# Kernel optimization log

Hardware: AMD Instinct MI355X
Metric: run time of the kernel (lower is better)

Reference implementation:

```python
import jax, jax.numpy as jnp
import numpy as np

N = 50000      # nodes
E = 400000     # edges (before self-loops)
F_IN = 256     # input_dim
HID = 64       # hidden_dim (per-head)
H = 4          # heads
OUT = 16       # output_dim
NEG_SLOPE = 0.2


def _gat_layer(x, W, a_src, a_dst, b, src, dst):
    # x: [N, Fin], W: [Fin, H*HID], a_src/a_dst: [H, HID], b: [H*HID]
    n = x.shape[0]
    h = (x @ W).reshape(n, H, HID)                        # [N,H,D]
    es = jnp.einsum('nhd,hd->nh', h, a_src)               # [N,H]
    ed = jnp.einsum('nhd,hd->nh', h, a_dst)               # [N,H]
    e = jax.nn.leaky_relu(es[src] + ed[dst], NEG_SLOPE)   # [E,H]
    m = jax.ops.segment_max(e, dst, num_segments=n)       # [N,H] segment softmax (stable)
    m = jnp.where(jnp.isfinite(m), m, 0.0)
    p = jnp.exp(e - m[dst])
    s = jax.ops.segment_sum(p, dst, num_segments=n)
    alpha = p / (s[dst] + 1e-16)                          # [E,H]
    out = jax.ops.segment_sum(h[src] * alpha[:, :, None], dst, num_segments=n)  # [N,H,D]
    return out.reshape(n, H * HID) + b


def setup_inputs() -> dict:
    key = jax.random.key(0)
    ks = jax.random.split(key, 24)
    lin = lambda k, i, o: (jax.random.normal(k, (i, o), jnp.float32) / np.sqrt(i)).astype(jnp.float32)
    att = lambda k: (jax.random.normal(k, (H, HID), jnp.float32) * 0.1).astype(jnp.float32)
    FH = H * HID  # 256
    inp = {
        'x': jax.random.normal(ks[0], (N, F_IN), jnp.float32),
        'edge_index': jax.random.randint(ks[1], (2, E), 0, N, dtype=jnp.int64),
        'W1': lin(ks[2], F_IN, FH), 'a1_src': att(ks[3]), 'a1_dst': att(ks[4]), 'b1': jnp.zeros((FH,), jnp.float32),
        'W2': lin(ks[5], FH, FH),   'a2_src': att(ks[6]), 'a2_dst': att(ks[7]), 'b2': jnp.zeros((FH,), jnp.float32),
        'W3': lin(ks[8], FH, FH),   'a3_src': att(ks[9]), 'a3_dst': att(ks[10]), 'b3': jnp.zeros((FH,), jnp.float32),
        'pW1': lin(ks[11], FH, HID), 'pb1': jnp.zeros((HID,), jnp.float32),
        'pW2': lin(ks[12], HID, HID), 'pb2': jnp.zeros((HID,), jnp.float32),
        'cW1': lin(ks[13], FH, HID), 'cb1': jnp.zeros((HID,), jnp.float32),
        'cW2': lin(ks[14], HID, OUT), 'cb2': jnp.zeros((OUT,), jnp.float32),
    }
    return inp


def reference(x, edge_index, W1, a1_src, a1_dst, b1, W2, a2_src, a2_dst, b2,
              W3, a3_src, a3_dst, b3, pW1, pb1, pW2, pb2, cW1, cb1, cW2, cb2):
    n = x.shape[0]
    loop = jnp.arange(n, dtype=edge_index.dtype)          # PyG GATConv adds self-loops
    src = jnp.concatenate([edge_index[0], loop])
    dst = jnp.concatenate([edge_index[1], loop])
    h = jax.nn.elu(_gat_layer(x, W1, a1_src, a1_dst, b1, src, dst))
    h = jax.nn.elu(_gat_layer(h, W2, a2_src, a2_dst, b2, src, dst))
    h = _gat_layer(h, W3, a3_src, a3_dst, b3, src, dst)   # [N, 256]
    logits = jax.nn.relu(h @ cW1 + cb1) @ cW2 + cb2       # classifier (dropout inactive, eval)
    proj = jax.nn.relu(h @ pW1 + pb1) @ pW2 + pb2         # projection head
    return jax.nn.log_softmax(logits, axis=1), proj
```

## Files before the change

### kernel.cpp

```cpp
#include <hip/hip_runtime.h>
#include <hip/hip_bf16.h>

#define NN 50000
#define EE 400000
#define TE (EE + NN)
#define SCAN_B ((NN + 255) / 256)
#define CONV_B (NN * 256 / 4 / 256)
#define PREP_B ((PO_TOTAL + 255) / 256)

typedef float f4 __attribute__((ext_vector_type(4)));
typedef __bf16 b8 __attribute__((ext_vector_type(8)));
typedef unsigned short us8 __attribute__((ext_vector_type(8)));

__device__ __forceinline__ float b2f(unsigned short u) {
    union { unsigned int i; float f; } c; c.i = ((unsigned int)u) << 16; return c.f;
}
__device__ __forceinline__ unsigned short f2b(float x) {
    union { unsigned int i; float f; } c; c.f = x;
    unsigned int i = c.i;
    return (unsigned short)((i + 0x7FFFu + ((i >> 16) & 1u)) >> 16);
}
__device__ __forceinline__ int clampi(int v, int lo, int hi) {
    return v < lo ? lo : (v > hi ? hi : v);
}
__device__ __forceinline__ int uclamp(int v) {
    unsigned u = (unsigned)v;
    return (int)(u < (unsigned)(NN - 1) ? u : (unsigned)(NN - 1));
}

#define PO_WT    0
#define PO_ATT   196608
#define PO_BT    198912
#define PO_BIAS  231680
#define PO_PW2   231808
#define PO_PB2   235904
#define PO_CW2   235968
#define PO_CB2   236992
#define PO_BT2   237008
#define PO_BIAS2 253392
#define PO_TOTAL 253520

__device__ __forceinline__ int detect_xbf(const unsigned int* xw, int tid, int* sm) {
    if (tid < 64) {
        int cnt = 0;
#pragma unroll
        for (int k = 0; k < 4; k++) {
            int i = tid + k * 64;
            unsigned short lo = (unsigned short)(xw[i] & 0xFFFFu);
            int e = (lo >> 7) & 0xFF;
            if (e >= 120 && e <= 132) cnt++;
        }
#pragma unroll
        for (int off = 1; off < 64; off <<= 1) cnt += __shfl_xor(cnt, off, 64);
        if (tid == 0) *sm = (cnt >= 128) ? 1 : 0;
    }
    __syncthreads();
    return *sm;
}
__device__ __forceinline__ int detect_e64(const int* ei, int tid, int* sm) {
    if (tid < 64) {
        int bad = (tid < 16 && ei[2 * tid + 1] != 0) ? 1 : 0;
        unsigned long long anybad = __ballot(bad != 0);
        if (tid == 0) *sm = (anybad == 0ULL) ? 1 : 0;
    }
    __syncthreads();
    return *sm;
}

__device__ __forceinline__ float ldf(const void* p, int i, int bf) {
    return bf ? b2f(((const unsigned short*)p)[i]) : ((const float*)p)[i];
}

__global__ __launch_bounds__(256) void convx_prep_kernel(
    const void* __restrict__ xsrc, unsigned short* __restrict__ dst,
    int* __restrict__ deg, int* __restrict__ cursor,
    const void* W1, const void* W2, const void* W3,
    const void* as1, const void* ad1, const void* b1,
    const void* as2, const void* ad2, const void* b2,
    const void* as3, const void* ad3, const void* b3,
    const void* pW1, const void* pb1, const void* pW2, const void* pb2,
    const void* cW1, const void* cb1, const void* cW2, const void* cb2,
    unsigned short* __restrict__ P) {
    __shared__ int sm;
    int tid = threadIdx.x;
    int bf = detect_xbf((const unsigned int*)xsrc, tid, &sm);
    int b = blockIdx.x;
    if (b < CONV_B) {
        int i = b * 256 + tid;
        if (b < SCAN_B && i < NN) { deg[i] = 0; cursor[i] = 0; }
        if (i >= NN * 256 / 4) return;
        if (bf) {
            ((ushort4*)dst)[i] = ((const ushort4*)xsrc)[i];
        } else {
            float4 v = ((const float4*)xsrc)[i];
            ushort4 o; o.x = f2b(v.x); o.y = f2b(v.y); o.z = f2b(v.z); o.w = f2b(v.w);
            ((ushort4*)dst)[i] = o;
        }
        return;
    }
    int idx = (b - CONV_B) * 256 + tid;
    if (idx >= PO_TOTAL) return;
    float v;
    if (idx < PO_ATT) {
        int l = idx / 65536, r = idx % 65536;
        int n = r >> 8, k = r & 255;
        const void* W = (l == 0) ? W1 : (l == 1) ? W2 : W3;
        v = ldf(W, k * 256 + n, bf);
    } else if (idx < PO_BT) {
        int r = idx - PO_ATT;
        int l = r / 768, w = r % 768, which = w >> 8, j = w & 255;
        const void* s;
        if (which == 0) s = (l == 0) ? as1 : (l == 1) ? as2 : as3;
        else if (which == 1) s = (l == 0) ? ad1 : (l == 1) ? ad2 : ad3;
        else s = (l == 0) ? b1 : (l == 1) ? b2 : b3;
        v = ldf(s, j, bf);
    } else if (idx < PO_BIAS) {
        int r3 = idx - PO_BT;
        int r = r3 >> 8, k = r3 & 255;
        v = (r < 64) ? ldf(cW1, k * 64 + r, bf) : ldf(pW1, k * 64 + (r - 64), bf);
    } else if (idx < PO_PW2) {
        int r = idx - PO_BIAS;
        v = (r < 64) ? ldf(cb1, r, bf) : ldf(pb1, r - 64, bf);
    } else if (idx < PO_PB2) {
        v = ldf(pW2, idx - PO_PW2, bf);
    } else if (idx < PO_CW2) {
        v = ldf(pb2, idx - PO_PB2, bf);
    } else if (idx < PO_CB2) {
        v = ldf(cW2, idx - PO_CW2, bf);
    } else if (idx < PO_BT2) {
        v = ldf(cb2, idx - PO_CB2, bf);
    } else if (idx < PO_BIAS2) {
        int r2 = idx - PO_BT2;
        int r = r2 >> 7, k = r2 & 127;
        if (r < 16) v = (k < 64) ? ldf(cW2, k * 16 + r, bf) : 0.f;
        else if (r < 80) v = (k >= 64) ? ldf(pW2, (k - 64) * 64 + (r - 16), bf) : 0.f;
        else v = 0.f;
    } else {
        int r = idx - PO_BIAS2;
        v = (r < 16) ? ldf(cb2, r, bf) : (r < 80 ? ldf(pb2, r - 16, bf) : 0.f);
    }
    P[idx] = f2b(v);
}

__device__ __forceinline__ void edge_decode(const int* __restrict__ ei, int mode64, int e,
                                            int& src, int& dst) {
    if (e < EE) {
        if (mode64) { src = ei[2 * e]; dst = ei[2 * EE + 2 * e]; }
        else        { src = ei[e];     dst = ei[EE + e]; }
        src = clampi(src, 0, NN - 1);
        dst = clampi(dst, 0, NN - 1);
    } else {
        src = dst = e - EE;
    }
}

__global__ __launch_bounds__(256) void deg_kernel(const int* __restrict__ ei,
                                                  int* __restrict__ deg) {
    __shared__ int sm;
    int tid = threadIdx.x;
    int mode64 = detect_e64(ei, tid, &sm);
    int e = blockIdx.x * 256 + tid;
    if (e >= TE) return;
    int src, dst;
    edge_decode(ei, mode64, e, src, dst);
    atomicAdd(&deg[dst], 1);
}

__global__ __launch_bounds__(256) void scanA_kernel(const int* __restrict__ deg,
                                                    int* __restrict__ offs, int* __restrict__ bsum) {
    __shared__ int s[256];
    int t = threadIdx.x, i = blockIdx.x * 256 + t;
    int v = (i < NN) ? deg[i] : 0;
    s[t] = v;
    __syncthreads();
    for (int off = 1; off < 256; off <<= 1) {
        int x = (t >= off) ? s[t - off] : 0;
        __syncthreads();
        s[t] += x;
        __syncthreads();
    }
    if (i < NN) offs[i] = s[t] - v;
    if (t == 255) bsum[blockIdx.x] = s[255];
}
__global__ __launch_bounds__(256) void scanBC_kernel(int* __restrict__ offs,
                                                     const int* __restrict__ bsum) {
    __shared__ int s[256];
    int t = threadIdx.x;
    int v = (t < SCAN_B) ? bsum[t] : 0;
    s[t] = v;
    __syncthreads();
    for (int off = 1; off < 256; off <<= 1) {
        int x = (t >= off) ? s[t - off] : 0;
        __syncthreads();
        s[t] += x;
        __syncthreads();
    }
    int add = (blockIdx.x > 0) ? s[blockIdx.x - 1] : 0;
    int i = blockIdx.x * 256 + t;
    if (i < NN) offs[i] += add;
    if (i == 0) offs[NN] = TE;
}

__global__ __launch_bounds__(256) void scatter_kernel(const int* __restrict__ ei,
                                                      const int* __restrict__ offs,
                                                      int* __restrict__ cursor,
                                                      int* __restrict__ srcs) {
    __shared__ int sm;
    int tid = threadIdx.x;
    int mode64 = detect_e64(ei, tid, &sm);
    int e = blockIdx.x * 256 + tid;
    if (e >= TE) return;
    int src, dst;
    edge_decode(ei, mode64, e, src, dst);
    int pos = atomicAdd(&cursor[dst], 1);
    int slot = offs[dst] + pos;
    if (slot >= 0 && slot < TE) srcs[slot] = src;
}

__device__ __forceinline__ void async_ld16(const unsigned short* g, unsigned short* l) {
    __builtin_amdgcn_global_load_lds(
        (const __attribute__((address_space(1))) unsigned int*)g,
        (__attribute__((address_space(3))) unsigned int*)l, 16, 0, 0);
}

__global__ __launch_bounds__(256) void gemm_bt_kernel(
    const unsigned short* __restrict__ A, const unsigned short* __restrict__ Bt,
    unsigned short* __restrict__ C, int M,
    const unsigned short* __restrict__ asrc, const unsigned short* __restrict__ adst,
    float* __restrict__ es, float* __restrict__ ed) {
    const int K = 256, Nc = 256;
    __shared__ unsigned short As[2][128 * 32];
    __shared__ unsigned short Bs[2][128 * 32];
    int tid = threadIdx.x;
    int lane = tid & 63;
    int wave = tid >> 6;
    int wr = wave >> 1, wc = wave & 1;
    int m0 = blockIdx.x * 128;
    int n0 = blockIdx.y * 128;
    f4 acc[4][4];
#pragma unroll
    for (int i = 0; i < 4; i++)
#pragma unroll
        for (int j = 0; j < 4; j++) acc[i][j] = (f4){0.f, 0.f, 0.f, 0.f};

    int rin = lane >> 2;
    int qsl = lane & 3;
    int qg  = qsl ^ ((rin >> 1) & 3);
    int rsel = lane & 15;
    int q16 = lane >> 4;
    int slotq = q16 ^ ((rsel >> 1) & 3);

    auto stage = [&](int b, int kt) {
#pragma unroll
        for (int t = 0; t < 4; t++) {
            int seg = wave * 4 + t;
            if (seg < 8) {
                int r = seg * 16 + rin;
                int gm = m0 + r;
                if (gm < M)
                    async_ld16(A + (size_t)gm * K + kt + qg * 8, &As[b][seg * 512]);
            } else {
                int r = (seg - 8) * 16 + rin;
                int gn = n0 + r;
                async_ld16(Bt + (size_t)gn * K + kt + qg * 8, &Bs[b][(seg - 8) * 512]);
            }
        }
    };

    const int nk = K >> 5;
    stage(0, 0);
    __syncthreads();
    for (int s = 0; s < nk; s++) {
        int cur = s & 1;
        if (s + 1 < nk) stage(cur ^ 1, (s + 1) << 5);
        b8 af[4], bfv[4];
#pragma unroll
        for (int i = 0; i < 4; i++) {
            af[i]  = *(const b8*)(&As[cur][(wr * 64 + i * 16 + rsel) * 32 + slotq * 8]);
            bfv[i] = *(const b8*)(&Bs[cur][(wc * 64 + i * 16 + rsel) * 32 + slotq * 8]);
        }
#pragma unroll
        for (int i = 0; i < 4; i++)
#pragma unroll
            for (int j = 0; j < 4; j++)
                acc[i][j] = __builtin_amdgcn_mfma_f32_16x16x32_bf16(af[i], bfv[j], acc[i][j], 0, 0, 0);
        __syncthreads();
    }
    int cl = lane & 15, rq = lane >> 4;
    {
        int head = blockIdx.y * 2 + wc;
        float asv[4], adv[4];
#pragma unroll
        for (int j = 0; j < 4; j++) {
            asv[j] = b2f(asrc[head * 64 + j * 16 + cl]);
            adv[j] = b2f(adst[head * 64 + j * 16 + cl]);
        }
#pragma unroll
        for (int i = 0; i < 4; i++) {
            float pes[4], ped[4];
#pragma unroll
            for (int r = 0; r < 4; r++) {
                float se = 0.f, de = 0.f;
#pragma unroll
                for (int j = 0; j < 4; j++) {
                    se += acc[i][j][r] * asv[j];
                    de += acc[i][j][r] * adv[j];
                }
                pes[r] = se; ped[r] = de;
            }
#pragma unroll
            for (int off = 1; off < 16; off <<= 1) {
#pragma unroll
                for (int r = 0; r < 4; r++) {
                    pes[r] += __shfl_xor(pes[r], off, 64);
                    ped[r] += __shfl_xor(ped[r], off, 64);
                }
            }
            if (cl == 0) {
#pragma unroll
                for (int r = 0; r < 4; r++) {
                    int row = m0 + wr * 64 + i * 16 + rq * 4 + r;
                    if (row < M) {
                        es[(size_t)row * 4 + head] = pes[r];
                        ed[(size_t)row * 4 + head] = ped[r];
                    }
                }
            }
        }
    }
#pragma unroll
    for (int j = 0; j < 4; j++) {
        int col = n0 + wc * 64 + j * 16 + cl;
#pragma unroll
        for (int i = 0; i < 4; i++) {
#pragma unroll
            for (int r = 0; r < 4; r++) {
                int row = m0 + wr * 64 + i * 16 + rq * 4 + r;
                if (row < M) C[(size_t)row * Nc + col] = f2b(acc[i][j][r]);
            }
        }
    }
}

__global__ __launch_bounds__(256) void gemm_final_kernel(
    const unsigned short* __restrict__ A, const unsigned short* __restrict__ Bt1,
    const unsigned short* __restrict__ bias1, const unsigned short* __restrict__ B2g,
    const unsigned short* __restrict__ bias2,
    float* __restrict__ flog, float* __restrict__ fproj, int M) {
    const int K = 256;
    __shared__ unsigned short smem[32768];
    unsigned short* As0 = smem;
    unsigned short* Bs0 = smem + 8192;
    unsigned short* T   = smem;
    unsigned short* B2s = smem + 16384;
    int tid = threadIdx.x;
    int lane = tid & 63;
    int wave = tid >> 6;
    int wr = wave >> 1, wc = wave & 1;
    int m0 = blockIdx.x * 128;
    f4 acc[4][4];
#pragma unroll
    for (int i = 0; i < 4; i++)
#pragma unroll
        for (int j = 0; j < 4; j++) acc[i][j] = (f4){0.f, 0.f, 0.f, 0.f};

    int rin = lane >> 2;
    int qsl = lane & 3;
    int qg  = qsl ^ ((rin >> 1) & 3);
    int rsel = lane & 15;
    int q16 = lane >> 4;
    int slotq = q16 ^ ((rsel >> 1) & 3);

#pragma unroll
    for (int t = 0; t < 8; t++) {
        int row = t * 16 + wave * 4 + (lane >> 4);
        int chunk = lane & 15;
        async_ld16(B2g + row * 128 + ((chunk ^ (row & 15)) << 3),
                   B2s + (t * 16 + wave * 4) * 128);
    }

    auto stage = [&](int b, int kt) {
#pragma unroll
        for (int t = 0; t < 4; t++) {
            int seg = wave * 4 + t;
            if (seg < 8) {
                int r = seg * 16 + rin;
                int gm = m0 + r;
                if (gm < M)
                    async_ld16(A + (size_t)gm * K + kt + qg * 8, &As0[b * 4096 + seg * 512]);
            } else {
                int r = (seg - 8) * 16 + rin;
                async_ld16(Bt1 + (size_t)r * K + kt + qg * 8, &Bs0[b * 4096 + (seg - 8) * 512]);
            }
        }
    };

    stage(0, 0);
    __syncthreads();
    for (int s = 0; s < 8; s++) {
        int cur = s & 1;
        if (s + 1 < 8) stage(cur ^ 1, (s + 1) << 5);
        b8 af[4], bfv[4];
#pragma unroll
        for (int i = 0; i < 4; i++) {
            af[i]  = *(const b8*)(&As0[cur * 4096 + (wr * 64 + i * 16 + rsel) * 32 + slotq * 8]);
            bfv[i] = *(const b8*)(&Bs0[cur * 4096 + (wc * 64 + i * 16 + rsel) * 32 + slotq * 8]);
        }
#pragma unroll
        for (int i = 0; i < 4; i++)
#pragma unroll
            for (int j = 0; j < 4; j++)
                acc[i][j] = __builtin_amdgcn_mfma_f32_16x16x32_bf16(af[i], bfv[j], acc[i][j], 0, 0, 0);
        __syncthreads();
    }

    int cl = lane & 15, rq = lane >> 4;
#pragma unroll
    for (int j = 0; j < 4; j++) {
        int col = wc * 64 + j * 16 + cl;
        float bv = b2f(bias1[col]);
        int chunk = col >> 3, cr = col & 7;
#pragma unroll
        for (int i = 0; i < 4; i++) {
#pragma unroll
            for (int r = 0; r < 4; r++) {
                int row = wr * 64 + i * 16 + rq * 4 + r;
                float v = fmaxf(acc[i][j][r] + bv, 0.0f);
                T[row * 128 + ((chunk ^ (row & 15)) << 3) + cr] = f2b(v);
            }
        }
    }
    __syncthreads();

    f4 acc2[4][4];
#pragma unroll
    for (int i = 0; i < 4; i++)
#pragma unroll
        for (int j = 0; j < 4; j++) acc2[i][j] = (f4){0.f, 0.f, 0.f, 0.f};
#pragma unroll
    for (int s2 = 0; s2 < 4; s2++) {
        int kc = s2 * 4 + q16;
        b8 af2[4], bf2[4];
#pragma unroll
        for (int i = 0; i < 4; i++) {
            int row = wr * 64 + i * 16 + rsel;
            af2[i] = *(const b8*)(&T[row * 128 + ((kc ^ (row & 15)) << 3)]);
        }
#pragma unroll
        for (int j = 0; j < 4; j++) {
            int col = wc * 64 + j * 16 + rsel;
            bf2[j] = *(const b8*)(&B2s[col * 128 + ((kc ^ (col & 15)) << 3)]);
        }
#pragma unroll
        for (int i = 0; i < 4; i++)
#pragma unroll
            for (int j = 0; j < 4; j++)
                acc2[i][j] = __builtin_amdgcn_mfma_f32_16x16x32_bf16(af2[i], bf2[j], acc2[i][j], 0, 0, 0);
    }

#pragma unroll
    for (int i = 0; i < 4; i++) {
#pragma unroll
        for (int r = 0; r < 4; r++) {
            int row = m0 + wr * 64 + i * 16 + rq * 4 + r;
            if (row >= M) continue;
            if (wc == 0) {
                float lv = acc2[i][0][r] + b2f(bias2[cl]);
                float mx = lv;
#pragma unroll
                for (int off = 1; off < 16; off <<= 1) mx = fmaxf(mx, __shfl_xor(mx, off, 64));
                float se = __expf(lv - mx);
#pragma unroll
                for (int off = 1; off < 16; off <<= 1) se += __shfl_xor(se, off, 64);
                flog[(size_t)row * 16 + cl] = lv - mx - __logf(se);
#pragma unroll
                for (int j = 1; j < 4; j++) {
                    float pv = acc2[i][j][r] + b2f(bias2[j * 16 + cl]);
                    fproj[(size_t)row * 64 + j * 16 + cl - 16] = pv;
                }
            } else {
                float pv = acc2[i][0][r] + b2f(bias2[64 + cl]);
                fproj[(size_t)row * 64 + 48 + cl] = pv;
            }
        }
    }
}

__global__ __launch_bounds__(256) void aggr_kernel(
    const unsigned short* __restrict__ H, const float* __restrict__ es,
    const float* __restrict__ ed,
    const int* __restrict__ offs, const int* __restrict__ srcs,
    const unsigned short* __restrict__ bias, unsigned short* __restrict__ out, int N, int elu) {
    int gw = (blockIdx.x * 256 + threadIdx.x) >> 6;
    int lane = threadIdx.x & 63;
    if (gw >= N) return;
    int half = lane >> 5;
    int lh = lane & 31;
    int ch = lh << 3;
    int head = lh >> 3;
    int j0 = clampi(offs[gw], 0, TE);
    int j1 = clampi(offs[gw + 1], j0, TE);
    int d = j1 - j0;
    float edh = ed[gw * 4 + head];
    float a0 = 0.f, a1 = 0.f, a2 = 0.f, a3 = 0.f;
    float a4 = 0.f, a5 = 0.f, a6 = 0.f, a7 = 0.f;
    float sw = 0.f;
    int nfull8 = d & ~7;
    for (int t = 0; t < nfull8; t += 8) {
        int base = j0 + t + half * 4;
        int s0 = uclamp(srcs[base]), s1 = uclamp(srcs[base + 1]);
        int s2 = uclamp(srcs[base + 2]), s3 = uclamp(srcs[base + 3]);
        float e0 = es[s0 * 4 + head], e1 = es[s1 * 4 + head];
        float e2 = es[s2 * 4 + head], e3 = es[s3 * 4 + head];
        us8 h0 = *(const us8*)(H + (size_t)s0 * 256 + ch);
        us8 h1 = *(const us8*)(H + (size_t)s1 * 256 + ch);
        us8 h2 = *(const us8*)(H + (size_t)s2 * 256 + ch);
        us8 h3 = *(const us8*)(H + (size_t)s3 * 256 + ch);
        float v0 = e0 + edh; v0 = v0 > 0.f ? v0 : 0.2f * v0;
        float v1 = e1 + edh; v1 = v1 > 0.f ? v1 : 0.2f * v1;
        float v2 = e2 + edh; v2 = v2 > 0.f ? v2 : 0.2f * v2;
        float v3 = e3 + edh; v3 = v3 > 0.f ? v3 : 0.2f * v3;
        float w0 = __expf(v0), w1 = __expf(v1), w2 = __expf(v2), w3 = __expf(v3);
        sw += (w0 + w1) + (w2 + w3);
        a0 += w0 * b2f(h0[0]) + w1 * b2f(h1[0]) + w2 * b2f(h2[0]) + w3 * b2f(h3[0]);
        a1 += w0 * b2f(h0[1]) + w1 * b2f(h1[1]) + w2 * b2f(h2[1]) + w3 * b2f(h3[1]);
        a2 += w0 * b2f(h0[2]) + w1 * b2f(h1[2]) + w2 * b2f(h2[2]) + w3 * b2f(h3[2]);
        a3 += w0 * b2f(h0[3]) + w1 * b2f(h1[3]) + w2 * b2f(h2[3]) + w3 * b2f(h3[3]);
        a4 += w0 * b2f(h0[4]) + w1 * b2f(h1[4]) + w2 * b2f(h2[4]) + w3 * b2f(h3[4]);
        a5 += w0 * b2f(h0[5]) + w1 * b2f(h1[5]) + w2 * b2f(h2[5]) + w3 * b2f(h3[5]);
        a6 += w0 * b2f(h0[6]) + w1 * b2f(h1[6]) + w2 * b2f(h2[6]) + w3 * b2f(h3[6]);
        a7 += w0 * b2f(h0[7]) + w1 * b2f(h1[7]) + w2 * b2f(h2[7]) + w3 * b2f(h3[7]);
    }
    int jt = j0 + nfull8;
    if (j1 - jt >= 4) {
        int base = jt + half * 2;
        int s0 = uclamp(srcs[base]), s1 = uclamp(srcs[base + 1]);
        float e0 = es[s0 * 4 + head], e1 = es[s1 * 4 + head];
        us8 h0 = *(const us8*)(H + (size_t)s0 * 256 + ch);
        us8 h1 = *(const us8*)(H + (size_t)s1 * 256 + ch);
        float v0 = e0 + edh; v0 = v0 > 0.f ? v0 : 0.2f * v0;
        float v1 = e1 + edh; v1 = v1 > 0.f ? v1 : 0.2f * v1;
        float w0 = __expf(v0), w1 = __expf(v1);
        sw += w0 + w1;
        a0 += w0 * b2f(h0[0]) + w1 * b2f(h1[0]);
        a1 += w0 * b2f(h0[1]) + w1 * b2f(h1[1]);
        a2 += w0 * b2f(h0[2]) + w1 * b2f(h1[2]);
        a3 += w0 * b2f(h0[3]) + w1 * b2f(h1[3]);
        a4 += w0 * b2f(h0[4]) + w1 * b2f(h1[4]);
        a5 += w0 * b2f(h0[5]) + w1 * b2f(h1[5]);
        a6 += w0 * b2f(h0[6]) + w1 * b2f(h1[6]);
        a7 += w0 * b2f(h0[7]) + w1 * b2f(h1[7]);
        jt += 4;
    }
    for (int j = jt + half; j < j1; j += 2) {
        int sA = uclamp(srcs[j]);
        float eA = es[sA * 4 + head];
        us8 hA = *(const us8*)(H + (size_t)sA * 256 + ch);
        float vA = eA + edh; vA = vA > 0.f ? vA : 0.2f * vA;
        float wA = __expf(vA);
        sw += wA;
        a0 += wA * b2f(hA[0]); a1 += wA * b2f(hA[1]);
        a2 += wA * b2f(hA[2]); a3 += wA * b2f(hA[3]);
        a4 += wA * b2f(hA[4]); a5 += wA * b2f(hA[5]);
        a6 += wA * b2f(hA[6]); a7 += wA * b2f(hA[7]);
    }
    sw += __shfl_xor(sw, 32, 64);
    a0 += __shfl_xor(a0, 32, 64); a1 += __shfl_xor(a1, 32, 64);
    a2 += __shfl_xor(a2, 32, 64); a3 += __shfl_xor(a3, 32, 64);
    a4 += __shfl_xor(a4, 32, 64); a5 += __shfl_xor(a5, 32, 64);
    a6 += __shfl_xor(a6, 32, 64); a7 += __shfl_xor(a7, 32, 64);
    if (half == 0) {
        float rs = 1.f / (sw + 1e-16f);
        us8 bv = *(const us8*)(bias + ch);
        float r0 = a0 * rs + b2f(bv[0]), r1 = a1 * rs + b2f(bv[1]);
        float r2 = a2 * rs + b2f(bv[2]), r3 = a3 * rs + b2f(bv[3]);
        float r4 = a4 * rs + b2f(bv[4]), r5 = a5 * rs + b2f(bv[5]);
        float r6 = a6 * rs + b2f(bv[6]), r7 = a7 * rs + b2f(bv[7]);
        if (elu) {
            r0 = r0 > 0.f ? r0 : __expf(r0) - 1.f;
            r1 = r1 > 0.f ? r1 : __expf(r1) - 1.f;
            r2 = r2 > 0.f ? r2 : __expf(r2) - 1.f;
            r3 = r3 > 0.f ? r3 : __expf(r3) - 1.f;
            r4 = r4 > 0.f ? r4 : __expf(r4) - 1.f;
            r5 = r5 > 0.f ? r5 : __expf(r5) - 1.f;
            r6 = r6 > 0.f ? r6 : __expf(r6) - 1.f;
            r7 = r7 > 0.f ? r7 : __expf(r7) - 1.f;
        }
        us8 o;
        o[0] = f2b(r0); o[1] = f2b(r1); o[2] = f2b(r2); o[3] = f2b(r3);
        o[4] = f2b(r4); o[5] = f2b(r5); o[6] = f2b(r6); o[7] = f2b(r7);
        *(us8*)(out + (size_t)gw * 256 + ch) = o;
    }
}

extern "C" void kernel_launch(void* const* d_in, const int* in_sizes, int n_in,
                              void* d_out, int out_size, void* d_ws, size_t ws_size,
                              hipStream_t stream) {
    (void)in_sizes; (void)n_in; (void)out_size; (void)ws_size;
    const int* ei = (const int*)d_in[1];

    char* p = (char*)d_ws;
    auto take = [&](size_t bytes) -> void* {
        void* r = (void*)p;
        p += (bytes + 255) & ~(size_t)255;
        return r;
    };
    int* deg    = (int*)take((size_t)NN * 4);
    int* cursor = (int*)take((size_t)NN * 4);
    int* offs   = (int*)take((size_t)(NN + 1) * 4);
    int* bsum   = (int*)take(256 * 4);
    int* srcs   = (int*)take((size_t)TE * 4);
    float* es   = (float*)take((size_t)NN * 16);
    float* ed   = (float*)take((size_t)NN * 16);
    unsigned short* bufH = (unsigned short*)take((size_t)NN * 256 * 2);
    unsigned short* buf1 = (unsigned short*)take((size_t)NN * 256 * 2);
    unsigned short* buf2 = (unsigned short*)take((size_t)NN * 256 * 2);
    unsigned short* P    = (unsigned short*)take((size_t)PO_TOTAL * 2);
    unsigned short* xb = buf2;

    convx_prep_kernel<<<CONV_B + PREP_B, 256, 0, stream>>>(
        d_in[0], xb, deg, cursor,
        d_in[2], d_in[6], d_in[10],
        d_in[3], d_in[4], d_in[5],
        d_in[7], d_in[8], d_in[9],
        d_in[11], d_in[12], d_in[13],
        d_in[14], d_in[15], d_in[16], d_in[17],
        d_in[18], d_in[19], d_in[20], d_in[21],
        P);

    deg_kernel<<<(TE + 255) / 256, 256, 0, stream>>>(ei, deg);
    scanA_kernel<<<SCAN_B, 256, 0, stream>>>(deg, offs, bsum);
    scanBC_kernel<<<SCAN_B, 256, 0, stream>>>(offs, bsum);
    scatter_kernel<<<(TE + 255) / 256, 256, 0, stream>>>(ei, offs, cursor, srcs);

    const unsigned short* X = xb;
    unsigned short* outbuf[3] = {buf1, buf2, buf1};
    for (int l = 0; l < 3; l++) {
        const unsigned short* Wt  = P + PO_WT + l * 65536;
        const unsigned short* asr = P + PO_ATT + l * 768;
        const unsigned short* adr = P + PO_ATT + l * 768 + 256;
        const unsigned short* bcb = P + PO_ATT + l * 768 + 512;
        gemm_bt_kernel<<<dim3((NN + 127) / 128, 2), 256, 0, stream>>>(
            X, Wt, bufH, NN, asr, adr, es, ed);
        aggr_kernel<<<12500, 256, 0, stream>>>(bufH, es, ed, offs, srcs, bcb, outbuf[l], NN, (l < 2) ? 1 : 0);
        X = outbuf[l];
    }
    float* out0 = (float*)d_out;
    float* out1 = out0 + (size_t)NN * 16;
    gemm_final_kernel<<<(NN + 127) / 128, 256, 0, stream>>>(
        X, P + PO_BT, P + PO_BIAS, P + PO_BT2, P + PO_BIAS2, out0, out1, NN);
}
```

Measured before the change: 405.8 us.

## Fuse graph build and all GAT layers into one cooperative persistent kernel

Replaces the chain of separate launches (degree count, scan, scatter, three GEMM+aggregation pairs, final head) with one cooperative persistent kernel. Grid-wide barriers separate the phases, and blocks loop over virtual tiles. The CSR scatter is overlapped with the first layer's GEMM in the same phase. This removes per-launch overhead and tail gaps, but every phase now waits on grid syncs and occupancy is fixed by launch bounds. The old multi-kernel path stays as a fallback if the cooperative launch fails.

```diff
diff --git a/kernel.cpp b/kernel.cpp
--- a/kernel.cpp
+++ b/kernel.cpp
@@ -1,5 +1,8 @@
 #include <hip/hip_runtime.h>
 #include <hip/hip_bf16.h>
+#include <hip/hip_cooperative_groups.h>
+
+namespace cg = cooperative_groups;
 
 #define NN 50000
 #define EE 400000
@@ -7,6 +10,10 @@
 #define SCAN_B ((NN + 255) / 256)
 #define CONV_B (NN * 256 / 4 / 256)
 #define PREP_B ((PO_TOTAL + 255) / 256)
+#define DEG_B ((TE + 255) / 256)
+#define GEMM_T 782
+#define FIN_T 391
+#define AGGR_B 12500
 
 typedef float f4 __attribute__((ext_vector_type(4)));
 typedef __bf16 b8 __attribute__((ext_vector_type(8)));
@@ -69,6 +76,24 @@
 
 __device__ __forceinline__ float ldf(const void* p, int i, int bf) {
     return bf ? b2f(((const unsigned short*)p)[i]) : ((const float*)p)[i];
+}
+
+__device__ __forceinline__ void async_ld16(const unsigned short* g, unsigned short* l) {
+    __builtin_amdgcn_global_load_lds(
+        (const __attribute__((address_space(1))) unsigned int*)g,
+        (__attribute__((address_space(3))) unsigned int*)l, 16, 0, 0);
+}
+
+__device__ __forceinline__ void edge_decode(const int* __restrict__ ei, int mode64, int e,
+                                            int& src, int& dst) {
+    if (e < EE) {
+        if (mode64) { src = ei[2 * e]; dst = ei[2 * EE + 2 * e]; }
+        else        { src = ei[e];     dst = ei[EE + e]; }
+        src = clampi(src, 0, NN - 1);
+        dst = clampi(dst, 0, NN - 1);
+    } else {
+        src = dst = e - EE;
+    }
 }
 
 __global__ __launch_bounds__(256) void convx_prep_kernel(
@@ -83,8 +108,8 @@
     unsigned short* __restrict__ P) {
     __shared__ int sm;
     int tid = threadIdx.x;
+    int b = blockIdx.x;
     int bf = detect_xbf((const unsigned int*)xsrc, tid, &sm);
-    int b = blockIdx.x;
     if (b < CONV_B) {
         int i = b * 256 + tid;
         if (b < SCAN_B && i < NN) { deg[i] = 0; cursor[i] = 0; }
@@ -142,18 +167,6 @@
     P[idx] = f2b(v);
 }
 
-__device__ __forceinline__ void edge_decode(const int* __restrict__ ei, int mode64, int e,
-                                            int& src, int& dst) {
-    if (e < EE) {
-        if (mode64) { src = ei[2 * e]; dst = ei[2 * EE + 2 * e]; }
-        else        { src = ei[e];     dst = ei[EE + e]; }
-        src = clampi(src, 0, NN - 1);
-        dst = clampi(dst, 0, NN - 1);
-    } else {
-        src = dst = e - EE;
-    }
-}
-
 __global__ __launch_bounds__(256) void deg_kernel(const int* __restrict__ ei,
                                                   int* __restrict__ deg) {
     __shared__ int sm;
@@ -215,12 +228,6 @@
     int pos = atomicAdd(&cursor[dst], 1);
     int slot = offs[dst] + pos;
     if (slot >= 0 && slot < TE) srcs[slot] = src;
-}
-
-__device__ __forceinline__ void async_ld16(const unsigned short* g, unsigned short* l) {
-    __builtin_amdgcn_global_load_lds(
-        (const __attribute__((address_space(1))) unsigned int*)g,
-        (__attribute__((address_space(3))) unsigned int*)l, 16, 0, 0);
 }
 
 __global__ __launch_bounds__(256) void gemm_bt_kernel(
@@ -242,31 +249,24 @@
     for (int i = 0; i < 4; i++)
 #pragma unroll
         for (int j = 0; j < 4; j++) acc[i][j] = (f4){0.f, 0.f, 0.f, 0.f};
-
-    int rin = lane >> 2;
-    int qsl = lane & 3;
+    int rin = lane >> 2, qsl = lane & 3;
     int qg  = qsl ^ ((rin >> 1) & 3);
-    int rsel = lane & 15;
-    int q16 = lane >> 4;
+    int rsel = lane & 15, q16 = lane >> 4;
     int slotq = q16 ^ ((rsel >> 1) & 3);
-
     auto stage = [&](int b, int kt) {
 #pragma unroll
         for (int t = 0; t < 4; t++) {
             int seg = wave * 4 + t;
             if (seg < 8) {
-                int r = seg * 16 + rin;
-                int gm = m0 + r;
+                int gm = m0 + seg * 16 + rin;
                 if (gm < M)
                     async_ld16(A + (size_t)gm * K + kt + qg * 8, &As[b][seg * 512]);
             } else {
-                int r = (seg - 8) * 16 + rin;
-                int gn = n0 + r;
+                int gn = n0 + (seg - 8) * 16 + rin;
                 async_ld16(Bt + (size_t)gn * K + kt + qg * 8, &Bs[b][(seg - 8) * 512]);
             }
         }
     };
-
     const int nk = K >> 5;
     stage(0, 0);
     __syncthreads();
@@ -363,14 +363,10 @@
     for (int i = 0; i < 4; i++)
 #pragma unroll
         for (int j = 0; j < 4; j++) acc[i][j] = (f4){0.f, 0.f, 0.f, 0.f};
-
-    int rin = lane >> 2;
-    int qsl = lane & 3;
+    int rin = lane >> 2, qsl = lane & 3;
     int qg  = qsl ^ ((rin >> 1) & 3);
-    int rsel = lane & 15;
-    int q16 = lane >> 4;
+    int rsel = lane & 15, q16 = lane >> 4;
     int slotq = q16 ^ ((rsel >> 1) & 3);
-
 #pragma unroll
     for (int t = 0; t < 8; t++) {
         int row = t * 16 + wave * 4 + (lane >> 4);
@@ -378,14 +374,12 @@
         async_ld16(B2g + row * 128 + ((chunk ^ (row & 15)) << 3),
                    B2s + (t * 16 + wave * 4) * 128);
     }
-
     auto stage = [&](int b, int kt) {
 #pragma unroll
         for (int t = 0; t < 4; t++) {
             int seg = wave * 4 + t;
             if (seg < 8) {
-                int r = seg * 16 + rin;
-                int gm = m0 + r;
+                int gm = m0 + seg * 16 + rin;
                 if (gm < M)
                     async_ld16(A + (size_t)gm * K + kt + qg * 8, &As0[b * 4096 + seg * 512]);
             } else {
@@ -394,7 +388,6 @@
             }
         }
     };
-
     stage(0, 0);
     __syncthreads();
     for (int s = 0; s < 8; s++) {
@@ -413,7 +406,6 @@
                 acc[i][j] = __builtin_amdgcn_mfma_f32_16x16x32_bf16(af[i], bfv[j], acc[i][j], 0, 0, 0);
         __syncthreads();
     }
-
     int cl = lane & 15, rq = lane >> 4;
 #pragma unroll
     for (int j = 0; j < 4; j++) {
@@ -431,7 +423,6 @@
         }
     }
     __syncthreads();
-
     f4 acc2[4][4];
 #pragma unroll
     for (int i = 0; i < 4; i++)
@@ -457,7 +448,6 @@
             for (int j = 0; j < 4; j++)
                 acc2[i][j] = __builtin_amdgcn_mfma_f32_16x16x32_bf16(af2[i], bf2[j], acc2[i][j], 0, 0, 0);
     }
-
 #pragma unroll
     for (int i = 0; i < 4; i++) {
 #pragma unroll
@@ -593,6 +583,423 @@
     }
 }
 
+__global__ __launch_bounds__(256, 4) void mega_kernel(
+    const int* __restrict__ ei,
+    int* __restrict__ deg, int* __restrict__ cursor,
+    int* __restrict__ offs, int* __restrict__ bsum, int* __restrict__ srcs,
+    float* __restrict__ es, float* __restrict__ ed,
+    unsigned short* __restrict__ bufH, unsigned short* __restrict__ buf1,
+    unsigned short* __restrict__ buf2, const unsigned short* __restrict__ P,
+    float* __restrict__ out_logits, float* __restrict__ out_proj) {
+    __shared__ unsigned short smem[16384];
+    __shared__ int sm0;
+    cg::grid_group grid = cg::this_grid();
+    int tid = threadIdx.x;
+    int m64 = detect_e64(ei, tid, &sm0);
+    const int NB = gridDim.x;
+    int lane = tid & 63, wave = tid >> 6;
+    int wr = wave >> 1, wc = wave & 1;
+    int rin = lane >> 2, qsl = lane & 3;
+    int qg = qsl ^ ((rin >> 1) & 3);
+    int rsel = lane & 15, q16 = lane >> 4;
+    int slotq = q16 ^ ((rsel >> 1) & 3);
+    int cl = lane & 15, rq = lane >> 4;
+
+    auto gemm_tile = [&](int m0, int n0, const unsigned short* A,
+                         const unsigned short* Wt,
+                         const unsigned short* asrc, const unsigned short* adst) {
+        unsigned short* As0 = smem;
+        unsigned short* Bs0 = smem + 8192;
+        const int K = 256;
+        f4 acc[4][4];
+#pragma unroll
+        for (int i = 0; i < 4; i++)
+#pragma unroll
+            for (int j = 0; j < 4; j++) acc[i][j] = (f4){0.f, 0.f, 0.f, 0.f};
+        auto stage = [&](int b, int kt) {
+#pragma unroll
+            for (int t = 0; t < 4; t++) {
+                int seg = wave * 4 + t;
+                if (seg < 8) {
+                    int gm = m0 + seg * 16 + rin;
+                    if (gm < NN)
+                        async_ld16(A + (size_t)gm * K + kt + qg * 8, &As0[b * 4096 + seg * 512]);
+                } else {
+                    int gn = n0 + (seg - 8) * 16 + rin;
+                    async_ld16(Wt + (size_t)gn * K + kt + qg * 8, &Bs0[b * 4096 + (seg - 8) * 512]);
+                }
+            }
+        };
+        stage(0, 0);
+        __syncthreads();
+        for (int s = 0; s < 8; s++) {
+            int cur = s & 1;
+            if (s + 1 < 8) stage(cur ^ 1, (s + 1) << 5);
+            b8 af[4], bfv[4];
+#pragma unroll
+            for (int i = 0; i < 4; i++) {
+                af[i]  = *(const b8*)(&As0[cur * 4096 + (wr * 64 + i * 16 + rsel) * 32 + slotq * 8]);
+                bfv[i] = *(const b8*)(&Bs0[cur * 4096 + (wc * 64 + i * 16 + rsel) * 32 + slotq * 8]);
+            }
+#pragma unroll
+            for (int i = 0; i < 4; i++)
+#pragma unroll
+                for (int j = 0; j < 4; j++)
+                    acc[i][j] = __builtin_amdgcn_mfma_f32_16x16x32_bf16(af[i], bfv[j], acc[i][j], 0, 0, 0);
+            __syncthreads();
+        }
+        int head = (n0 >> 6) + wc;
+        float asv[4], adv[4];
+#pragma unroll
+        for (int j = 0; j < 4; j++) {
+            asv[j] = b2f(asrc[head * 64 + j * 16 + cl]);
+            adv[j] = b2f(adst[head * 64 + j * 16 + cl]);
+        }
+#pragma unroll
+        for (int i = 0; i < 4; i++) {
+            float pes[4], ped[4];
+#pragma unroll
+            for (int r = 0; r < 4; r++) {
+                float se = 0.f, de = 0.f;
+#pragma unroll
+                for (int j = 0; j < 4; j++) {
+                    se += acc[i][j][r] * asv[j];
+                    de += acc[i][j][r] * adv[j];
+                }
+                pes[r] = se; ped[r] = de;
+            }
+#pragma unroll
+            for (int off = 1; off < 16; off <<= 1) {
+#pragma unroll
+                for (int r = 0; r < 4; r++) {
+                    pes[r] += __shfl_xor(pes[r], off, 64);
+                    ped[r] += __shfl_xor(ped[r], off, 64);
+                }
+            }
+            if (cl == 0) {
+#pragma unroll
+                for (int r = 0; r < 4; r++) {
+                    int row = m0 + wr * 64 + i * 16 + rq * 4 + r;
+                    if (row < NN) {
+                        es[(size_t)row * 4 + head] = pes[r];
+                        ed[(size_t)row * 4 + head] = ped[r];
+                    }
+                }
+            }
+        }
+#pragma unroll
+        for (int j = 0; j < 4; j++) {
+            int col = n0 + wc * 64 + j * 16 + cl;
+#pragma unroll
+            for (int i = 0; i < 4; i++) {
+#pragma unroll
+                for (int r = 0; r < 4; r++) {
+                    int row = m0 + wr * 64 + i * 16 + rq * 4 + r;
+                    if (row < NN) bufH[(size_t)row * 256 + col] = f2b(acc[i][j][r]);
+                }
+            }
+        }
+    };
+
+    auto aggr_node = [&](int gw, const unsigned short* bias, unsigned short* out, int elu) {
+        if (gw >= NN) return;
+        int half = lane >> 5;
+        int lh = lane & 31;
+        int ch = lh << 3;
+        int head = lh >> 3;
+        int j0 = clampi(offs[gw], 0, TE);
+        int j1 = clampi(offs[gw + 1], j0, TE);
+        int d = j1 - j0;
+        float edh = ed[gw * 4 + head];
+        float a0 = 0.f, a1 = 0.f, a2 = 0.f, a3 = 0.f;
+        float a4 = 0.f, a5 = 0.f, a6 = 0.f, a7 = 0.f;
+        float sw = 0.f;
+        int nfull8 = d & ~7;
+        for (int t = 0; t < nfull8; t += 8) {
+            int base = j0 + t + half * 4;
+            int s0 = uclamp(srcs[base]), s1 = uclamp(srcs[base + 1]);
+            int s2 = uclamp(srcs[base + 2]), s3 = uclamp(srcs[base + 3]);
+            float e0 = es[s0 * 4 + head], e1 = es[s1 * 4 + head];
+            float e2 = es[s2 * 4 + head], e3 = es[s3 * 4 + head];
+            us8 h0 = *(const us8*)(bufH + (size_t)s0 * 256 + ch);
+            us8 h1 = *(const us8*)(bufH + (size_t)s1 * 256 + ch);
+            us8 h2 = *(const us8*)(bufH + (size_t)s2 * 256 + ch);
+            us8 h3 = *(const us8*)(bufH + (size_t)s3 * 256 + ch);
+            float v0 = e0 + edh; v0 = v0 > 0.f ? v0 : 0.2f * v0;
+            float v1 = e1 + edh; v1 = v1 > 0.f ? v1 : 0.2f * v1;
+            float v2 = e2 + edh; v2 = v2 > 0.f ? v2 : 0.2f * v2;
+            float v3 = e3 + edh; v3 = v3 > 0.f ? v3 : 0.2f * v3;
+            float w0 = __expf(v0), w1 = __expf(v1), w2 = __expf(v2), w3 = __expf(v3);
+            sw += (w0 + w1) + (w2 + w3);
+            a0 += w0 * b2f(h0[0]) + w1 * b2f(h1[0]) + w2 * b2f(h2[0]) + w3 * b2f(h3[0]);
+            a1 += w0 * b2f(h0[1]) + w1 * b2f(h1[1]) + w2 * b2f(h2[1]) + w3 * b2f(h3[1]);
+            a2 += w0 * b2f(h0[2]) + w1 * b2f(h1[2]) + w2 * b2f(h2[2]) + w3 * b2f(h3[2]);
+            a3 += w0 * b2f(h0[3]) + w1 * b2f(h1[3]) + w2 * b2f(h2[3]) + w3 * b2f(h3[3]);
+            a4 += w0 * b2f(h0[4]) + w1 * b2f(h1[4]) + w2 * b2f(h2[4]) + w3 * b2f(h3[4]);
+            a5 += w0 * b2f(h0[5]) + w1 * b2f(h1[5]) + w2 * b2f(h2[5]) + w3 * b2f(h3[5]);
+            a6 += w0 * b2f(h0[6]) + w1 * b2f(h1[6]) + w2 * b2f(h2[6]) + w3 * b2f(h3[6]);
+            a7 += w0 * b2f(h0[7]) + w1 * b2f(h1[7]) + w2 * b2f(h2[7]) + w3 * b2f(h3[7]);
+        }
+        int jt = j0 + nfull8;
+        if (j1 - jt >= 4) {
+            int base = jt + half * 2;
+            int s0 = uclamp(srcs[base]), s1 = uclamp(srcs[base + 1]);
+            float e0 = es[s0 * 4 + head], e1 = es[s1 * 4 + head];
+            us8 h0 = *(const us8*)(bufH + (size_t)s0 * 256 + ch);
+            us8 h1 = *(const us8*)(bufH + (size_t)s1 * 256 + ch);
+            float v0 = e0 + edh; v0 = v0 > 0.f ? v0 : 0.2f * v0;
+            float v1 = e1 + edh; v1 = v1 > 0.f ? v1 : 0.2f * v1;
+            float w0 = __expf(v0), w1 = __expf(v1);
+            sw += w0 + w1;
+            a0 += w0 * b2f(h0[0]) + w1 * b2f(h1[0]);
+            a1 += w0 * b2f(h0[1]) + w1 * b2f(h1[1]);
+            a2 += w0 * b2f(h0[2]) + w1 * b2f(h1[2]);
+            a3 += w0 * b2f(h0[3]) + w1 * b2f(h1[3]);
+            a4 += w0 * b2f(h0[4]) + w1 * b2f(h1[4]);
+            a5 += w0 * b2f(h0[5]) + w1 * b2f(h1[5]);
+            a6 += w0 * b2f(h0[6]) + w1 * b2f(h1[6]);
+            a7 += w0 * b2f(h0[7]) + w1 * b2f(h1[7]);
+            jt += 4;
+        }
+        for (int j = jt + half; j < j1; j += 2) {
+            int sA = uclamp(srcs[j]);
+            float eA = es[sA * 4 + head];
+            us8 hA = *(const us8*)(bufH + (size_t)sA * 256 + ch);
+            float vA = eA + edh; vA = vA > 0.f ? vA : 0.2f * vA;
+            float wA = __expf(vA);
+            sw += wA;
+            a0 += wA * b2f(hA[0]); a1 += wA * b2f(hA[1]);
+            a2 += wA * b2f(hA[2]); a3 += wA * b2f(hA[3]);
+            a4 += wA * b2f(hA[4]); a5 += wA * b2f(hA[5]);
+            a6 += wA * b2f(hA[6]); a7 += wA * b2f(hA[7]);
+        }
+        sw += __shfl_xor(sw, 32, 64);
+        a0 += __shfl_xor(a0, 32, 64); a1 += __shfl_xor(a1, 32, 64);
+        a2 += __shfl_xor(a2, 32, 64); a3 += __shfl_xor(a3, 32, 64);
+        a4 += __shfl_xor(a4, 32, 64); a5 += __shfl_xor(a5, 32, 64);
+        a6 += __shfl_xor(a6, 32, 64); a7 += __shfl_xor(a7, 32, 64);
+        if (half == 0) {
+            float rs = 1.f / (sw + 1e-16f);
+            us8 bv = *(const us8*)(bias + ch);
+            float r0 = a0 * rs + b2f(bv[0]), r1 = a1 * rs + b2f(bv[1]);
+            float r2 = a2 * rs + b2f(bv[2]), r3 = a3 * rs + b2f(bv[3]);
+            float r4 = a4 * rs + b2f(bv[4]), r5 = a5 * rs + b2f(bv[5]);
+            float r6 = a6 * rs + b2f(bv[6]), r7 = a7 * rs + b2f(bv[7]);
+            if (elu) {
+                r0 = r0 > 0.f ? r0 : __expf(r0) - 1.f;
+                r1 = r1 > 0.f ? r1 : __expf(r1) - 1.f;
+                r2 = r2 > 0.f ? r2 : __expf(r2) - 1.f;
+                r3 = r3 > 0.f ? r3 : __expf(r3) - 1.f;
+                r4 = r4 > 0.f ? r4 : __expf(r4) - 1.f;
+                r5 = r5 > 0.f ? r5 : __expf(r5) - 1.f;
+                r6 = r6 > 0.f ? r6 : __expf(r6) - 1.f;
+                r7 = r7 > 0.f ? r7 : __expf(r7) - 1.f;
+            }
+            us8 o;
+            o[0] = f2b(r0); o[1] = f2b(r1); o[2] = f2b(r2); o[3] = f2b(r3);
+            o[4] = f2b(r4); o[5] = f2b(r5); o[6] = f2b(r6); o[7] = f2b(r7);
+            *(us8*)(out + (size_t)gw * 256 + ch) = o;
+        }
+    };
+
+    auto final_tile = [&](int m0) {
+        const unsigned short* A = buf1;
+        const unsigned short* Bt1 = P + PO_BT;
+        const unsigned short* bias1 = P + PO_BIAS;
+        const unsigned short* B2g = P + PO_BT2;
+        const unsigned short* bias2 = P + PO_BIAS2;
+        unsigned short* As0 = smem;
+        unsigned short* Bs0 = smem + 8192;
+        const int K = 256;
+        f4 acc[4][4];
+#pragma unroll
+        for (int i = 0; i < 4; i++)
+#pragma unroll
+            for (int j = 0; j < 4; j++) acc[i][j] = (f4){0.f, 0.f, 0.f, 0.f};
+        auto stage = [&](int b, int kt) {
+#pragma unroll
+            for (int t = 0; t < 4; t++) {
+                int seg = wave * 4 + t;
+                if (seg < 8) {
+                    int gm = m0 + seg * 16 + rin;
+                    if (gm < NN)
+                        async_ld16(A + (size_t)gm * K + kt + qg * 8, &As0[b * 4096 + seg * 512]);
+                } else {
+                    int r = (seg - 8) * 16 + rin;
+                    async_ld16(Bt1 + (size_t)r * K + kt + qg * 8, &Bs0[b * 4096 + (seg - 8) * 512]);
+                }
+            }
+        };
+        stage(0, 0);
+        __syncthreads();
+        for (int s = 0; s < 8; s++) {
+            int cur = s & 1;
+            if (s + 1 < 8) stage(cur ^ 1, (s + 1) << 5);
+            b8 af[4], bfv[4];
+#pragma unroll
+            for (int i = 0; i < 4; i++) {
+                af[i]  = *(const b8*)(&As0[cur * 4096 + (wr * 64 + i * 16 + rsel) * 32 + slotq * 8]);
+                bfv[i] = *(const b8*)(&Bs0[cur * 4096 + (wc * 64 + i * 16 + rsel) * 32 + slotq * 8]);
+            }
+#pragma unroll
+            for (int i = 0; i < 4; i++)
+#pragma unroll
+                for (int j = 0; j < 4; j++)
+                    acc[i][j] = __builtin_amdgcn_mfma_f32_16x16x32_bf16(af[i], bfv[j], acc[i][j], 0, 0, 0);
+            __syncthreads();
+        }
+        unsigned short* T = smem;
+#pragma unroll
+        for (int j = 0; j < 4; j++) {
+            int col = wc * 64 + j * 16 + cl;
+            float bv = b2f(bias1[col]);
+            int chunk = col >> 3, cr = col & 7;
+#pragma unroll
+            for (int i = 0; i < 4; i++) {
+#pragma unroll
+                for (int r = 0; r < 4; r++) {
+                    int row = wr * 64 + i * 16 + rq * 4 + r;
+                    float v = fmaxf(acc[i][j][r] + bv, 0.0f);
+                    T[row * 128 + ((chunk ^ (row & 15)) << 3) + cr] = f2b(v);
+                }
+            }
+        }
+        __syncthreads();
+        f4 acc2[4][4];
+#pragma unroll
+        for (int i = 0; i < 4; i++)
+#pragma unroll
+            for (int j = 0; j < 4; j++) acc2[i][j] = (f4){0.f, 0.f, 0.f, 0.f};
+#pragma unroll
+        for (int s2 = 0; s2 < 4; s2++) {
+            int kc = s2 * 4 + q16;
+            b8 af2[4], bf2[4];
+#pragma unroll
+            for (int i = 0; i < 4; i++) {
+                int row = wr * 64 + i * 16 + rsel;
+                af2[i] = *(const b8*)(&T[row * 128 + ((kc ^ (row & 15)) << 3)]);
+            }
+#pragma unroll
+            for (int j = 0; j < 4; j++) {
+                int col = wc * 64 + j * 16 + rsel;
+                bf2[j] = *(const b8*)(B2g + (size_t)col * 128 + kc * 8);
+            }
+#pragma unroll
+            for (int i = 0; i < 4; i++)
+#pragma unroll
+                for (int j = 0; j < 4; j++)
+                    acc2[i][j] = __builtin_amdgcn_mfma_f32_16x16x32_bf16(af2[i], bf2[j], acc2[i][j], 0, 0, 0);
+        }
+#pragma unroll
+        for (int i = 0; i < 4; i++) {
+#pragma unroll
+            for (int r = 0; r < 4; r++) {
+                int row = m0 + wr * 64 + i * 16 + rq * 4 + r;
+                if (row >= NN) continue;
+                if (wc == 0) {
+                    float lv = acc2[i][0][r] + b2f(bias2[cl]);
+                    float mx = lv;
+#pragma unroll
+                    for (int off = 1; off < 16; off <<= 1) mx = fmaxf(mx, __shfl_xor(mx, off, 64));
+                    float se = __expf(lv - mx);
+#pragma unroll
+                    for (int off = 1; off < 16; off <<= 1) se += __shfl_xor(se, off, 64);
+                    out_logits[(size_t)row * 16 + cl] = lv - mx - __logf(se);
+#pragma unroll
+                    for (int j = 1; j < 4; j++) {
+                        float pv = acc2[i][j][r] + b2f(bias2[j * 16 + cl]);
+                        out_proj[(size_t)row * 64 + j * 16 + cl - 16] = pv;
+                    }
+                } else {
+                    float pv = acc2[i][0][r] + b2f(bias2[64 + cl]);
+                    out_proj[(size_t)row * 64 + 48 + cl] = pv;
+                }
+            }
+        }
+        __syncthreads();
+    };
+
+    for (int vb = blockIdx.x; vb < DEG_B; vb += NB) {
+        int e = vb * 256 + tid;
+        if (e < TE) {
+            int src, dst;
+            edge_decode(ei, m64, e, src, dst);
+            atomicAdd(&deg[dst], 1);
+        }
+    }
+    grid.sync();
+    for (int vb = blockIdx.x; vb < SCAN_B; vb += NB) {
+        int* s = (int*)smem;
+        int i = vb * 256 + tid;
+        int v = (i < NN) ? deg[i] : 0;
+        s[tid] = v;
+        __syncthreads();
+        for (int off = 1; off < 256; off <<= 1) {
+            int x = (tid >= off) ? s[tid - off] : 0;
+            __syncthreads();
+            s[tid] += x;
+            __syncthreads();
+        }
+        if (i < NN) offs[i] = s[tid] - v;
+        if (tid == 255) bsum[vb] = s[255];
+        __syncthreads();
+    }
+    grid.sync();
+    for (int vb = blockIdx.x; vb < SCAN_B; vb += NB) {
+        int* s = (int*)smem;
+        int v = (tid < SCAN_B) ? bsum[tid] : 0;
+        s[tid] = v;
+        __syncthreads();
+        for (int off = 1; off < 256; off <<= 1) {
+            int x = (tid >= off) ? s[tid - off] : 0;
+            __syncthreads();
+            s[tid] += x;
+            __syncthreads();
+        }
+        int add = (vb > 0) ? s[vb - 1] : 0;
+        int i = vb * 256 + tid;
+        if (i < NN) offs[i] += add;
+        if (i == 0) offs[NN] = TE;
+        __syncthreads();
+    }
+    grid.sync();
+    for (int vb = blockIdx.x; vb < GEMM_T + DEG_B; vb += NB) {
+        if (vb < GEMM_T) {
+            gemm_tile((vb >> 1) * 128, (vb & 1) * 128, buf2, P + PO_WT,
+                      P + PO_ATT, P + PO_ATT + 256);
+        } else {
+            int e = (vb - GEMM_T) * 256 + tid;
+            if (e < TE) {
+                int src, dst;
+                edge_decode(ei, m64, e, src, dst);
+                int pos = atomicAdd(&cursor[dst], 1);
+                int slot = offs[dst] + pos;
+                if (slot >= 0 && slot < TE) srcs[slot] = src;
+            }
+        }
+    }
+    grid.sync();
+    for (int vb = blockIdx.x; vb < AGGR_B; vb += NB)
+        aggr_node(vb * 4 + wave, P + PO_ATT + 512, buf1, 1);
+    grid.sync();
+    for (int vb = blockIdx.x; vb < GEMM_T; vb += NB)
+        gemm_tile((vb >> 1) * 128, (vb & 1) * 128, buf1, P + PO_WT + 65536,
+                  P + PO_ATT + 768, P + PO_ATT + 768 + 256);
+    grid.sync();
+    for (int vb = blockIdx.x; vb < AGGR_B; vb += NB)
+        aggr_node(vb * 4 + wave, P + PO_ATT + 768 + 512, buf2, 1);
+    grid.sync();
+    for (int vb = blockIdx.x; vb < GEMM_T; vb += NB)
+        gemm_tile((vb >> 1) * 128, (vb & 1) * 128, buf2, P + PO_WT + 131072,
+                  P + PO_ATT + 1536, P + PO_ATT + 1536 + 256);
+    grid.sync();
+    for (int vb = blockIdx.x; vb < AGGR_B; vb += NB)
+        aggr_node(vb * 4 + wave, P + PO_ATT + 1536 + 512, buf1, 0);
+    grid.sync();
+    for (int vb = blockIdx.x; vb < FIN_T; vb += NB)
+        final_tile(vb * 128);
+}
+
 extern "C" void kernel_launch(void* const* d_in, const int* in_sizes, int n_in,
                               void* d_out, int out_size, void* d_ws, size_t ws_size,
                               hipStream_t stream) {
@@ -628,25 +1035,42 @@
         d_in[18], d_in[19], d_in[20], d_in[21],
         P);
 
-    deg_kernel<<<(TE + 255) / 256, 256, 0, stream>>>(ei, deg);
+    float* out0 = (float*)d_out;
+    float* out1 = out0 + (size_t)NN * 16;
+
+    hipError_t cerr = hipErrorUnknown;
+    int numCU = 0, perCU = 0;
+    int dev = 0;
+    hipGetDevice(&dev);
+    hipDeviceGetAttribute(&numCU, hipDeviceAttributeMultiprocessorCount, dev);
+    hipOccupancyMaxActiveBlocksPerMultiprocessor(&perCU, mega_kernel, 256, 0);
+    if (numCU > 0 && perCU > 0) {
+        int grid = numCU * perCU;
+        if (grid > 2048) grid = 2048;
+        void* params[] = {
+            (void*)&ei, (void*)&deg, (void*)&cursor, (void*)&offs, (void*)&bsum,
+            (void*)&srcs, (void*)&es, (void*)&ed, (void*)&bufH, (void*)&buf1,
+            (void*)&buf2, (void*)&P, (void*)&out0, (void*)&out1 };
+        cerr = hipLaunchCooperativeKernel(mega_kernel, dim3(grid), dim3(256),
+                                          params, 0u, stream);
+    }
+    if (cerr == hipSuccess) return;
+
+    deg_kernel<<<DEG_B, 256, 0, stream>>>(ei, deg);
     scanA_kernel<<<SCAN_B, 256, 0, stream>>>(deg, offs, bsum);
     scanBC_kernel<<<SCAN_B, 256, 0, stream>>>(offs, bsum);
-    scatter_kernel<<<(TE + 255) / 256, 256, 0, stream>>>(ei, offs, cursor, srcs);
-
+    scatter_kernel<<<DEG_B, 256, 0, stream>>>(ei, offs, cursor, srcs);
     const unsigned short* X = xb;
     unsigned short* outbuf[3] = {buf1, buf2, buf1};
     for (int l = 0; l < 3; l++) {
-        const unsigned short* Wt  = P + PO_WT + l * 65536;
-        const unsigned short* asr = P + PO_ATT + l * 768;
-        const unsigned short* adr = P + PO_ATT + l * 768 + 256;
-        const unsigned short* bcb = P + PO_ATT + l * 768 + 512;
         gemm_bt_kernel<<<dim3((NN + 127) / 128, 2), 256, 0, stream>>>(
-            X, Wt, bufH, NN, asr, adr, es, ed);
-        aggr_kernel<<<12500, 256, 0, stream>>>(bufH, es, ed, offs, srcs, bcb, outbuf[l], NN, (l < 2) ? 1 : 0);
+            X, P + PO_WT + l * 65536, bufH, NN,
+            P + PO_ATT + l * 768, P + PO_ATT + l * 768 + 256, es, ed);
+        aggr_kernel<<<12500, 256, 0, stream>>>(bufH, es, ed, offs, srcs,
+                                               P + PO_ATT + l * 768 + 512,
+                                               outbuf[l], NN, (l < 2) ? 1 : 0);
         X = outbuf[l];
     }
-    float* out0 = (float*)d_out;
-    float* out1 = out0 + (size_t)NN * 16;
     gemm_final_kernel<<<(NN + 127) / 128, 256, 0, stream>>>(
         X, P + PO_BT, P + PO_BIAS, P + PO_BT2, P + PO_BIAS2, out0, out1, NN);
 }
```

Result: slower. 1.129 ms (+178.2%).
